# Kernel optimization log

Measured on AMD Instinct MI355X. Metric: run time of the kernel, lower is better.

## Reference

```python
import jax, jax.numpy as jnp
import numpy as np
import math

N_CLASSES = 1000
CODE_LENGTH = 1024
IN_FEATURES = 4096
BATCH = 512
MAX_PROB = 0.95
POWER = 1.0


def _hadamard(n):
    # Sylvester construction; n must be a power of 2.
    H = np.array([[1.0]], dtype=np.float64)
    while H.shape[0] < n:
        H = np.block([[H, H], [H, -H]])
    return H


def setup_inputs() -> dict:
    key = jax.random.key(0)
    k1, k2, k3 = jax.random.split(key, 3)
    x = jax.random.normal(k1, (BATCH, IN_FEATURES), dtype=jnp.float32)
    out_feat = CODE_LENGTH - 1  # single head: code_length//1 - 1
    # nn.Linear default init: U(-1/sqrt(fan_in), 1/sqrt(fan_in))
    bound = 1.0 / math.sqrt(IN_FEATURES)
    W = jax.random.uniform(k2, (out_feat, IN_FEATURES), dtype=jnp.float32, minval=-bound, maxval=bound)
    b = jax.random.uniform(k3, (out_feat,), dtype=jnp.float32, minval=-bound, maxval=bound)
    labels = jnp.asarray(_hadamard(CODE_LENGTH)[:N_CLASSES, 1:], dtype=jnp.float32)  # (C, L-1)
    eps = jnp.float32(CODE_LENGTH * math.pow((1.0 - MAX_PROB) / (MAX_PROB * (N_CLASSES - 1)), 1.0 / POWER))
    power = jnp.float32(POWER)
    return {"x": x, "W": W, "b": b, "labels": labels, "eps": eps, "power": power}


def reference(x, W, b, labels, eps, power):
    # Linear head: (B, in) @ (in, L-1) + b
    h = jnp.tanh(x @ W.T + b)                               # (B, L-1)
    # L1 distance to each Hadamard code row: (B, 1, L-1) vs (C, L-1)
    d = jnp.sum(jnp.abs(h[:, None, :] - labels), axis=-1)   # (B, C)
    d = jnp.maximum(d, eps)
    inv = 1.0 / jnp.power(d, power)                          # (B, C)
    return inv / jnp.sum(inv, axis=-1, keepdims=True)
```

## Files before the change

### kernel.cpp

```cpp
#include <hip/hip_runtime.h>

#define BATCH 512
#define INFEAT 4096
#define LOUT 1023
#define NCLS 1000
#define NPAD 1024
#define SPLITK 8

typedef __bf16 bf16x8 __attribute__((ext_vector_type(8)));
typedef float f32x4 __attribute__((ext_vector_type(4)));

__device__ __forceinline__ unsigned short f2bf(float a) {
    unsigned u = __builtin_bit_cast(unsigned, a);
    return (unsigned short)((u + 0x7fffu + ((u >> 16) & 1u)) >> 16);
}
__device__ __forceinline__ float bf2f(unsigned short u) {
    return __builtin_bit_cast(float, ((unsigned)u) << 16);
}
__device__ __forceinline__ uint4 pack8(float4 a, float4 b) {
    union { __bf16 h[8]; uint4 u; } r;
    r.h[0] = (__bf16)a.x; r.h[1] = (__bf16)a.y;
    r.h[2] = (__bf16)a.z; r.h[3] = (__bf16)a.w;
    r.h[4] = (__bf16)b.x; r.h[5] = (__bf16)b.y;
    r.h[6] = (__bf16)b.z; r.h[7] = (__bf16)b.w;
    return r.u;
}

__global__ __launch_bounds__(512, 1) void k_gemm(
    const float* __restrict__ x, const float* __restrict__ W,
    unsigned short* __restrict__ partial) {
    __shared__ unsigned char lds[65536];
    const int bid = blockIdx.x;
    const int work = (bid & 7) * 32 + (bid >> 3);
    const int bn = work & 7, bm = (work >> 3) & 3, sp = work >> 5;
    const int tid = threadIdx.x;
    const int wave = tid >> 6, lane = tid & 63;
    const int lrow = lane & 15, lgrp = lane >> 4;
    const int wr = wave >> 2, wc = wave & 3;
    const int arow0 = bm * 128, brow0 = bn * 128, chunk0 = sp * 8;

    const int p0 = tid, p1 = 512 + tid;
    const int row0 = p0 >> 3, jb0 = p0 & 7;
    const int row1 = p1 >> 3, jb1 = p1 & 7;

    f32x4 acc[4][2] = {};
    float4 sAa[4], sAb[4], sBa[4], sBb[4];

    auto LOADR = [&](int t, float4 (&aa)[4], float4 (&bb)[4]) {
        const size_t c0 = (size_t)(chunk0 + t) * 64;
        {
            const float4* q = (const float4*)(x + (size_t)(arow0 + row0) * INFEAT + c0 + jb0 * 8);
            aa[0] = q[0]; aa[1] = q[1];
        }
        {
            const float4* q = (const float4*)(x + (size_t)(arow0 + row1) * INFEAT + c0 + jb1 * 8);
            aa[2] = q[0]; aa[3] = q[1];
        }
        {
            int wrow = brow0 + row0;
            if (wrow < LOUT) {
                const float4* q = (const float4*)(W + (size_t)wrow * INFEAT + c0 + jb0 * 8);
                bb[0] = q[0]; bb[1] = q[1];
            } else {
                bb[0] = make_float4(0.f, 0.f, 0.f, 0.f);
                bb[1] = make_float4(0.f, 0.f, 0.f, 0.f);
            }
        }
        {
            int wrow = brow0 + row1;
            if (wrow < LOUT) {
                const float4* q = (const float4*)(W + (size_t)wrow * INFEAT + c0 + jb1 * 8);
                bb[2] = q[0]; bb[3] = q[1];
            } else {
                bb[2] = make_float4(0.f, 0.f, 0.f, 0.f);
                bb[3] = make_float4(0.f, 0.f, 0.f, 0.f);
            }
        }
    };

    auto WRITE = [&](int bsel, float4 (&aa)[4], float4 (&bb)[4]) {
        unsigned char* lA = lds + bsel * 32768;
        unsigned char* lB = lA + 16384;
        *(uint4*)(lA + row0 * 128 + ((jb0 ^ (row0 & 7)) * 16)) = pack8(aa[0], aa[1]);
        *(uint4*)(lA + row1 * 128 + ((jb1 ^ (row1 & 7)) * 16)) = pack8(aa[2], aa[3]);
        *(uint4*)(lB + row0 * 128 + ((jb0 ^ (row0 & 7)) * 16)) = pack8(bb[0], bb[1]);
        *(uint4*)(lB + row1 * 128 + ((jb1 ^ (row1 & 7)) * 16)) = pack8(bb[2], bb[3]);
    };

    auto COMPUTE = [&](int bsel) {
        const unsigned char* lA = lds + bsel * 32768;
        const unsigned char* lB = lA + 16384;
        __builtin_amdgcn_s_setprio(1);
#pragma unroll
        for (int ks = 0; ks < 2; ++ks) {
            int swz = ((ks * 4 + lgrp) ^ (lrow & 7)) * 16;
            bf16x8 a[4], b[2];
#pragma unroll
            for (int m = 0; m < 4; ++m)
                a[m] = *(const bf16x8*)(lA + (wr * 64 + m * 16 + lrow) * 128 + swz);
#pragma unroll
            for (int n = 0; n < 2; ++n)
                b[n] = *(const bf16x8*)(lB + (wc * 32 + n * 16 + lrow) * 128 + swz);
#pragma unroll
            for (int m = 0; m < 4; ++m)
#pragma unroll
                for (int n = 0; n < 2; ++n)
                    acc[m][n] = __builtin_amdgcn_mfma_f32_16x16x32_bf16(
                        a[m], b[n], acc[m][n], 0, 0, 0);
        }
        __builtin_amdgcn_s_setprio(0);
    };

    LOADR(0, sAa, sAb);
    LOADR(1, sBa, sBb);
    asm volatile("s_waitcnt vmcnt(8)" ::: "memory");
    __builtin_amdgcn_sched_barrier(0);
    WRITE(0, sAa, sAb);
    LOADR(2, sAa, sAb);
    asm volatile("s_waitcnt lgkmcnt(0)" ::: "memory");
    __builtin_amdgcn_sched_barrier(0);
    __builtin_amdgcn_s_barrier();

#define STEP(T, SA, SB, VMC)                                          \
    COMPUTE(T & 1);                                                   \
    asm volatile("s_waitcnt vmcnt(" #VMC ")" ::: "memory");           \
    __builtin_amdgcn_sched_barrier(0);                                \
    WRITE((T + 1) & 1, SA, SB);                                       \
    if ((T) <= 4) LOADR((T) + 3, SA, SB);                             \
    asm volatile("s_waitcnt lgkmcnt(0)" ::: "memory");                \
    __builtin_amdgcn_sched_barrier(0);                                \
    __builtin_amdgcn_s_barrier();

    STEP(0, sBa, sBb, 8)
    STEP(1, sAa, sAb, 8)
    STEP(2, sBa, sBb, 8)
    STEP(3, sAa, sAb, 8)
    STEP(4, sBa, sBb, 8)
    STEP(5, sAa, sAb, 8)
    STEP(6, sBa, sBb, 0)
    COMPUTE(1);
#undef STEP

    unsigned short* P = partial + (size_t)sp * (BATCH * NPAD);
#pragma unroll
    for (int m = 0; m < 4; ++m)
#pragma unroll
        for (int n = 0; n < 2; ++n)
#pragma unroll
            for (int reg = 0; reg < 4; ++reg) {
                int r = arow0 + wr * 64 + m * 16 + lgrp * 4 + reg;
                int c = brow0 + wc * 32 + n * 16 + lrow;
                P[(size_t)r * NPAD + c] = f2bf(acc[m][n][reg]);
            }
}

__global__ __launch_bounds__(256) void k_fused(const unsigned short* __restrict__ partial,
                                               const float* __restrict__ bias,
                                               const float* __restrict__ epsp,
                                               const float* __restrict__ powp,
                                               float* __restrict__ out) {
    __shared__ float g[1024];
    __shared__ float wsum[4];
    const int r = blockIdx.x, t = threadIdx.x;
    const int n0 = t * 4;

    f32x4 v = {0.0f, 0.0f, 0.0f, 0.0f};
#pragma unroll
    for (int s = 0; s < SPLITK; ++s) {
        ushort4 p = *(const ushort4*)(partial + ((size_t)s * BATCH + r) * NPAD + n0);
        v[0] += bf2f(p.x); v[1] += bf2f(p.y); v[2] += bf2f(p.z); v[3] += bf2f(p.w);
    }
    float bb[4];
    if (t < 255) {
        float4 b4 = *(const float4*)(bias + n0);
        bb[0] = b4.x; bb[1] = b4.y; bb[2] = b4.z; bb[3] = b4.w;
    } else {
        bb[0] = bias[1020]; bb[1] = bias[1021]; bb[2] = bias[1022]; bb[3] = 0.0f;
    }
    if (t == 0) g[0] = 0.0f;
#pragma unroll
    for (int j = 0; j < 4; ++j) {
        int n = n0 + j;
        if (n < LOUT) g[n + 1] = tanhf(v[j] + bb[j]);
    }
    __syncthreads();

#pragma unroll 1
    for (int s = 0; s < 10; ++s) {
        int st = 1 << s;
#pragma unroll
        for (int pp = 0; pp < 2; ++pp) {
            int p = t + pp * 256;
            int idx = ((p >> s) << (s + 1)) | (p & (st - 1));
            float a = g[idx], c = g[idx + st];
            g[idx] = a + c;
            g[idx + st] = a - c;
        }
        __syncthreads();
    }

    const float eps = *epsp, pw = *powp;
    float iv[4];
    float ss = 0.0f;
#pragma unroll
    for (int j = 0; j < 4; ++j) {
        int c = n0 + j;
        float d = fmaxf(1023.0f - g[c], eps);
        float q = (pw == 1.0f) ? (1.0f / d) : powf(d, -pw);
        if (c >= NCLS) q = 0.0f;
        iv[j] = q;
        ss += q;
    }
#pragma unroll
    for (int m = 32; m; m >>= 1) ss += __shfl_xor(ss, m, 64);
    if ((t & 63) == 0) wsum[t >> 6] = ss;
    __syncthreads();
    float sc = 1.0f / (wsum[0] + wsum[1] + wsum[2] + wsum[3]);

    if (n0 < NCLS) {
        float4 o;
        o.x = iv[0] * sc; o.y = iv[1] * sc; o.z = iv[2] * sc; o.w = iv[3] * sc;
        *(float4*)(out + (size_t)r * NCLS + n0) = o;
    }
}

extern "C" void kernel_launch(void* const* d_in, const int* in_sizes, int n_in,
                              void* d_out, int out_size, void* d_ws, size_t ws_size,
                              hipStream_t stream) {
    const float* x = (const float*)d_in[0];
    const float* W = (const float*)d_in[1];
    const float* b = (const float*)d_in[2];
    const float* epsp = (const float*)d_in[4];
    const float* powp = (const float*)d_in[5];
    float* out = (float*)d_out;

    unsigned char* ws = (unsigned char*)d_ws;
    unsigned short* partial = (unsigned short*)ws;

    k_gemm<<<256, 512, 0, stream>>>(x, W, partial);
    k_fused<<<512, 256, 0, stream>>>(partial, b, epsp, powp, out);
}
```

Measured before the change: 25.92 us.

## Restructure GEMM main loop to overlap LDS writes and global loads with MFMA

The split-K GEMM loop is restructured so each step first reads all LDS fragments for the current buffer, then issues the bf16 LDS writes for the next buffer and the next global loads, then runs the MFMAs, with the barrier at the end. Previously the MFMA compute finished before the write and load phase began, each separated by explicit vmcnt waits and sched_barriers. The aim is to hide LDS-write and global-load latency behind matrix math. It also removes the explicit vmcnt waits and scheduling barriers and leaves correct ordering to the compiler's inserted waits, which may serialize differently than intended.

```diff
diff --git a/kernel.cpp b/kernel.cpp
--- a/kernel.cpp
+++ b/kernel.cpp
@@ -39,9 +39,8 @@
     const int wr = wave >> 2, wc = wave & 3;
     const int arow0 = bm * 128, brow0 = bn * 128, chunk0 = sp * 8;
 
-    const int p0 = tid, p1 = 512 + tid;
-    const int row0 = p0 >> 3, jb0 = p0 & 7;
-    const int row1 = p1 >> 3, jb1 = p1 & 7;
+    const int row0 = tid >> 3, jb0 = tid & 7;
+    const int row1 = (512 + tid) >> 3, jb1 = tid & 7;
 
     f32x4 acc[4][2] = {};
     float4 sAa[4], sAb[4], sBa[4], sBb[4];
@@ -87,59 +86,52 @@
         *(uint4*)(lB + row1 * 128 + ((jb1 ^ (row1 & 7)) * 16)) = pack8(bb[2], bb[3]);
     };
 
-    auto COMPUTE = [&](int bsel) {
+    auto STEP_BODY = [&](int bsel, float4 (&aa)[4], float4 (&bb)[4],
+                         bool do_write, bool do_load, int tload) {
         const unsigned char* lA = lds + bsel * 32768;
         const unsigned char* lB = lA + 16384;
-        __builtin_amdgcn_s_setprio(1);
+        bf16x8 fa[2][4], fb[2][2];
 #pragma unroll
         for (int ks = 0; ks < 2; ++ks) {
             int swz = ((ks * 4 + lgrp) ^ (lrow & 7)) * 16;
-            bf16x8 a[4], b[2];
 #pragma unroll
             for (int m = 0; m < 4; ++m)
-                a[m] = *(const bf16x8*)(lA + (wr * 64 + m * 16 + lrow) * 128 + swz);
+                fa[ks][m] = *(const bf16x8*)(lA + (wr * 64 + m * 16 + lrow) * 128 + swz);
 #pragma unroll
             for (int n = 0; n < 2; ++n)
-                b[n] = *(const bf16x8*)(lB + (wc * 32 + n * 16 + lrow) * 128 + swz);
+                fb[ks][n] = *(const bf16x8*)(lB + (wc * 32 + n * 16 + lrow) * 128 + swz);
+        }
+        if (do_write) WRITE(bsel ^ 1, aa, bb);
+        if (do_load) LOADR(tload, aa, bb);
+        __builtin_amdgcn_s_setprio(1);
+#pragma unroll
+        for (int ks = 0; ks < 2; ++ks)
 #pragma unroll
             for (int m = 0; m < 4; ++m)
 #pragma unroll
                 for (int n = 0; n < 2; ++n)
                     acc[m][n] = __builtin_amdgcn_mfma_f32_16x16x32_bf16(
-                        a[m], b[n], acc[m][n], 0, 0, 0);
-        }
+                        fa[ks][m], fb[ks][n], acc[m][n], 0, 0, 0);
         __builtin_amdgcn_s_setprio(0);
+        asm volatile("s_waitcnt lgkmcnt(0)" ::: "memory");
+        __builtin_amdgcn_s_barrier();
     };
 
     LOADR(0, sAa, sAb);
     LOADR(1, sBa, sBb);
-    asm volatile("s_waitcnt vmcnt(8)" ::: "memory");
-    __builtin_amdgcn_sched_barrier(0);
     WRITE(0, sAa, sAb);
     LOADR(2, sAa, sAb);
     asm volatile("s_waitcnt lgkmcnt(0)" ::: "memory");
-    __builtin_amdgcn_sched_barrier(0);
     __builtin_amdgcn_s_barrier();
 
-#define STEP(T, SA, SB, VMC)                                          \
-    COMPUTE(T & 1);                                                   \
-    asm volatile("s_waitcnt vmcnt(" #VMC ")" ::: "memory");           \
-    __builtin_amdgcn_sched_barrier(0);                                \
-    WRITE((T + 1) & 1, SA, SB);                                       \
-    if ((T) <= 4) LOADR((T) + 3, SA, SB);                             \
-    asm volatile("s_waitcnt lgkmcnt(0)" ::: "memory");                \
-    __builtin_amdgcn_sched_barrier(0);                                \
-    __builtin_amdgcn_s_barrier();
-
-    STEP(0, sBa, sBb, 8)
-    STEP(1, sAa, sAb, 8)
-    STEP(2, sBa, sBb, 8)
-    STEP(3, sAa, sAb, 8)
-    STEP(4, sBa, sBb, 8)
-    STEP(5, sAa, sAb, 8)
-    STEP(6, sBa, sBb, 0)
-    COMPUTE(1);
-#undef STEP
+    STEP_BODY(0, sBa, sBb, true, true, 3);
+    STEP_BODY(1, sAa, sAb, true, true, 4);
+    STEP_BODY(0, sBa, sBb, true, true, 5);
+    STEP_BODY(1, sAa, sAb, true, true, 6);
+    STEP_BODY(0, sBa, sBb, true, true, 7);
+    STEP_BODY(1, sAa, sAb, true, false, 0);
+    STEP_BODY(0, sBa, sBb, true, false, 0);
+    STEP_BODY(1, sAa, sAb, false, false, 0);
 
     unsigned short* P = partial + (size_t)sp * (BATCH * NPAD);
 #pragma unroll
```

New measurement: 26.15 us. No clear change (+0.9%).
